# Kernel tuning notes

Measured on AMD Instinct MI355X. Metric: run time of the kernel, lower is better.

Reference implementation:

```python
import jax, jax.numpy as jnp
import numpy as np

N, E, B = 20000, 60000, 512
F_IN, ED, H, C = 7, 3, 4, 256
HC = H * C  # 1024
D_MODEL = 1024
EPS_BN = 1e-5


def setup_inputs() -> dict:
    key = jax.random.key(0)
    ks = jax.random.split(key, 24)
    s = 0.05
    inp = {
        'x': jax.random.normal(ks[0], (N, F_IN), jnp.float32),
        'edge_index': jax.random.randint(ks[1], (2, E), 0, N, jnp.int32),
        'edge_attr': jax.random.normal(ks[2], (E, ED), jnp.float32),
        'batch': jnp.sort(jax.random.randint(ks[3], (N,), 0, B, jnp.int32)),
        'w0': jax.random.normal(ks[4], (F_IN, HC), jnp.float32) * s,
        'w_rest': jax.random.normal(ks[5], (3, HC, HC), jnp.float32) * s,
        'w_edge': jax.random.normal(ks[6], (4, ED, HC), jnp.float32) * s,
        'att_src': jax.random.normal(ks[7], (4, H, C), jnp.float32) * s,
        'att_dst': jax.random.normal(ks[8], (4, H, C), jnp.float32) * s,
        'att_edge': jax.random.normal(ks[9], (4, H, C), jnp.float32) * s,
        'bias012': jax.random.normal(ks[10], (3, HC), jnp.float32) * s,
        'bias3': jax.random.normal(ks[11], (C,), jnp.float32) * s,
        'bn_gamma': jnp.ones((3, HC), jnp.float32),
        'bn_beta': jnp.zeros((3, HC), jnp.float32),
        'bn_mean': jnp.zeros((3, HC), jnp.float32),
        'bn_var': jnp.ones((3, HC), jnp.float32),
        'gate_w': jax.random.normal(ks[12], (C, 1), jnp.float32) * s,
        'gate_b': jnp.zeros((1,), jnp.float32),
        'proj_w': jax.random.normal(ks[13], (C, D_MODEL), jnp.float32) * s,
        'proj_b': jnp.zeros((D_MODEL,), jnp.float32),
    }
    return inp


def _gat_layer(x, ei, ea, W, We, a_s, a_d, a_e, bias, concat):
    # PyG GATConv with edge_dim, add_self_loops=True (fill_value='mean'), eval mode (no dropout)
    n = x.shape[0]
    sl = jnp.arange(n, dtype=ei.dtype)
    ea_mean = ea.mean(axis=0)
    ei = jnp.concatenate([ei, jnp.stack([sl, sl])], axis=1)            # [2, E+N]
    ea = jnp.concatenate([ea, jnp.broadcast_to(ea_mean, (n, ea.shape[1]))], axis=0)
    h = (x @ W).reshape(n, H, C)                                       # [N,H,C]
    alpha_src = jnp.einsum('nhc,hc->nh', h, a_s)
    alpha_dst = jnp.einsum('nhc,hc->nh', h, a_d)
    eh = (ea @ We).reshape(-1, H, C)
    alpha_e = jnp.einsum('ehc,hc->eh', eh, a_e)
    src, dst = ei[0], ei[1]
    alpha = jax.nn.leaky_relu(alpha_src[src] + alpha_dst[dst] + alpha_e, 0.2)  # [E+N,H]
    amax = jax.ops.segment_max(alpha, dst, num_segments=n)
    alpha = jnp.exp(alpha - amax[dst])
    denom = jax.ops.segment_sum(alpha, dst, num_segments=n)
    alpha = alpha / (denom[dst] + 1e-16)
    msg = h[src] * alpha[:, :, None]                                   # [E+N,H,C]
    out = jax.ops.segment_sum(msg, dst, num_segments=n)                # [N,H,C]
    out = out.reshape(n, H * C) if concat else out.mean(axis=1)
    return out + bias


def reference(x, edge_index, edge_attr, batch, w0, w_rest, w_edge, att_src, att_dst,
              att_edge, bias012, bias3, bn_gamma, bn_beta, bn_mean, bn_var,
              gate_w, gate_b, proj_w, proj_b):
    h = x
    for i in range(4):
        W = w0 if i == 0 else w_rest[i - 1]
        concat = i < 3
        b = bias012[i] if concat else bias3
        h = _gat_layer(h, edge_index, edge_attr, W, w_edge[i],
                       att_src[i], att_dst[i], att_edge[i], b, concat)
        if i < 3:
            # BatchNorm1d in eval mode, then ReLU (dropout is identity in eval)
            h = (h - bn_mean[i]) * (bn_gamma[i] / jnp.sqrt(bn_var[i] + EPS_BN)) + bn_beta[i]
            h = jax.nn.relu(h)
    # AttentionalAggregation: segment softmax over gate scores, weighted sum per graph
    gate = h @ gate_w + gate_b                                         # [N,1]
    gmax = jax.ops.segment_max(gate, batch, num_segments=B)
    g = jnp.exp(gate - gmax[batch])
    gsum = jax.ops.segment_sum(g, batch, num_segments=B)
    w = g / (gsum[batch] + 1e-16)
    graph = jax.ops.segment_sum(w * h, batch, num_segments=B)          # [B,256]
    return graph @ proj_w + proj_b                                     # [B,1024]
```

## Files before the change

kernel.cpp:

```cpp
#include <hip/hip_runtime.h>
#include <math.h>

#define NN 20000
#define NP 20480
#define EE 60000
#define BB 512
#define HC 1024
#define HH 4
#define CC 256

typedef _Float16 f16;
typedef f16 half8 __attribute__((ext_vector_type(8)));
typedef f16 f16x4 __attribute__((ext_vector_type(4)));
typedef float floatx4 __attribute__((ext_vector_type(4)));
typedef float floatx16 __attribute__((ext_vector_type(16)));

__device__ __forceinline__ size_t af_off(int n, int c) {
    int mblk = n >> 7, rr = n & 127;
    int iter = c >> 5, kc = c & 31;
    int kh = kc >> 4, kg = (kc >> 3) & 1, e = kc & 7;
    return ((((size_t)(mblk * 32 + iter) * 2 + kh) * 4 + (rr >> 5)) * 64 +
            (kg * 32 + (rr & 31))) * 8 + e;
}

__global__ void ehist_kernel(const float* __restrict__ ea, const int* __restrict__ ei,
                             float* sums, int* counts, int E_) {
    int e = blockIdx.x * 256 + threadIdx.x;
    float s0 = 0.f, s1 = 0.f, s2 = 0.f;
    if (e < E_) {
        atomicAdd(&counts[ei[E_ + e]], 1);
        s0 = ea[e * 3 + 0];
        s1 = ea[e * 3 + 1];
        s2 = ea[e * 3 + 2];
    }
    for (int o = 32; o; o >>= 1) {
        s0 += __shfl_down(s0, o);
        s1 += __shfl_down(s1, o);
        s2 += __shfl_down(s2, o);
    }
    if ((threadIdx.x & 63) == 0) {
        atomicAdd(&sums[0], s0);
        atomicAdd(&sums[1], s1);
        atomicAdd(&sums[2], s2);
    }
}

__global__ void scan1_kernel(const int* __restrict__ counts, int* __restrict__ partial,
                             int* __restrict__ psums, int n) {
    __shared__ int sdata[256];
    int t = threadIdx.x;
    int i = blockIdx.x * 256 + t;
    int v = (i < n) ? counts[i] : 0;
    sdata[t] = v;
    __syncthreads();
#pragma unroll
    for (int off = 1; off < 256; off <<= 1) {
        int tmp = (t >= off) ? sdata[t - off] : 0;
        __syncthreads();
        sdata[t] += tmp;
        __syncthreads();
    }
    if (i < n) partial[i] = sdata[t];
    if (t == 255) psums[blockIdx.x] = sdata[255];
}

__global__ void scan2_kernel(int* __restrict__ psums, int nb) {
    __shared__ int sdata[128];
    int t = threadIdx.x;
    sdata[t] = (t < nb) ? psums[t] : 0;
    __syncthreads();
#pragma unroll
    for (int off = 1; off < 128; off <<= 1) {
        int tmp = (t >= off) ? sdata[t - off] : 0;
        __syncthreads();
        sdata[t] += tmp;
        __syncthreads();
    }
    if (t < nb) psums[t] = (t == 0) ? 0 : sdata[t - 1];
}

__global__ void scan3_kernel(const int* __restrict__ partial, const int* __restrict__ psums,
                             int* __restrict__ indptr, int n) {
    int i = blockIdx.x * 256 + threadIdx.x;
    if (i == 0) indptr[0] = 0;
    if (i < n) indptr[i + 1] = partial[i] + psums[blockIdx.x];
}

__global__ void scatter_kernel(const int* __restrict__ ei, const int* __restrict__ indptr,
                               int* fill, int* sorted, int* sdst, int E_) {
    int e = blockIdx.x * 256 + threadIdx.x;
    if (e >= E_) return;
    int d = ei[E_ + e];
    int pos = indptr[d] + atomicAdd(&fill[d], 1);
    sorted[pos] = e;
    sdst[pos] = d;
}

__global__ void bptr_kernel(const int* __restrict__ batch, int* bptr, int n, int nb) {
    int i = blockIdx.x * 256 + threadIdx.x;
    if (i >= n) return;
    int b = batch[i];
    if (i == 0) {
        for (int bb = 0; bb <= b; bb++) bptr[bb] = 0;
    } else {
        int pb = batch[i - 1];
        if (pb != b) {
            for (int bb = pb + 1; bb <= b; bb++) bptr[bb] = i;
        }
    }
    if (i == n - 1) {
        for (int bb = b + 1; bb <= nb; bb++) bptr[bb] = n;
    }
}

__global__ void prep0_kernel(const float* __restrict__ w_rest, f16* __restrict__ Bf,
                             const float* __restrict__ att_src,
                             const float* __restrict__ att_dst,
                             const float* __restrict__ w0,
                             const float* __restrict__ bias012, const float* __restrict__ bn_g,
                             const float* __restrict__ bn_b, const float* __restrict__ bn_m,
                             const float* __restrict__ bn_v,
                             const float* __restrict__ w_edge,
                             const float* __restrict__ att_edge,
                             const float* __restrict__ ea_sums,
                             float* __restrict__ wsv, float* __restrict__ wdv,
                             float* __restrict__ w0s, float* __restrict__ w0d,
                             float2* __restrict__ bnss,
                             float* __restrict__ Mmat, float* __restrict__ ae_self,
                             float invE) {
    int bid = blockIdx.x;
    int t = threadIdx.x;
    if (bid < 768) {
        __shared__ float tile[64][65];
        int bx = (bid & 15) * 64;
        int by = ((bid >> 4) & 15) * 64;
        int l = bid >> 8;
        int tr = t >> 6, tc = t & 63;
#pragma unroll
        for (int i = 0; i < 16; i++) {
            int r = by + i * 4 + tr;
            tile[i * 4 + tr][tc] = w_rest[(size_t)l * 1048576 + (size_t)r * 1024 + bx + tc];
        }
        __syncthreads();
        f16* bl = Bf + (size_t)l * 1048576;
#pragma unroll
        for (int ii = 0; ii < 2; ii++) {
            int idx = ii * 256 + t;
            int nl = idx >> 3, kg8 = idx & 7;
            int n = bx + nl, k = by + kg8 * 8;
            half8 v;
#pragma unroll
            for (int e = 0; e < 8; e++) v[e] = (f16)tile[kg8 * 8 + e][nl];
            *(half8*)&bl[af_off(n, k)] = v;
        }
    } else if (bid < 3840) {
        int b = bid - 768;
        int l = b >> 10, k = b & 1023;
        int hp = t >> 6, lane = t & 63;
        int col = hp * 256 + lane * 4;
        const float* wrow = w_rest + (size_t)l * 1048576 + (size_t)k * 1024;
        float4 w4 = *(const float4*)&wrow[col];
        float4 a4 = *(const float4*)&att_src[(l + 1) * HC + col];
        float4 d4 = *(const float4*)&att_dst[(l + 1) * HC + col];
        float sp = w4.x * a4.x + w4.y * a4.y + w4.z * a4.z + w4.w * a4.w;
        float dp = w4.x * d4.x + w4.y * d4.y + w4.z * d4.z + w4.w * d4.w;
        for (int m = 1; m < 64; m <<= 1) {
            sp += __shfl_xor(sp, m);
            dp += __shfl_xor(dp, m);
        }
        if (lane == 0) {
            wsv[((size_t)l * 1024 + k) * 4 + hp] = sp;
            wdv[((size_t)l * 1024 + k) * 4 + hp] = dp;
        }
    } else if (bid < 3847) {
        int f = bid - 3840;
        int hp = t >> 6, lane = t & 63;
        int col = hp * 256 + lane * 4;
        float4 w4 = *(const float4*)&w0[f * HC + col];
        float4 a4 = *(const float4*)&att_src[col];
        float4 d4 = *(const float4*)&att_dst[col];
        float sp = w4.x * a4.x + w4.y * a4.y + w4.z * a4.z + w4.w * a4.w;
        float dp = w4.x * d4.x + w4.y * d4.y + w4.z * d4.z + w4.w * d4.w;
        for (int m = 1; m < 64; m <<= 1) {
            sp += __shfl_xor(sp, m);
            dp += __shfl_xor(dp, m);
        }
        if (lane == 0) {
            w0s[f * 4 + hp] = sp;
            w0d[f * 4 + hp] = dp;
        }
    } else if (bid < 3859) {
        int i = (bid - 3847) * 256 + t;
        if (i < 3 * HC) {
            float s = bn_g[i] * rsqrtf(bn_v[i] + 1e-5f);
            float2 o;
            o.x = s;
            o.y = (bias012[i] - bn_m[i]) * s + bn_b[i];
            bnss[i] = o;
        }
    } else {
        __shared__ float red[256];
        __shared__ float Ms[12];
        int l = bid - 3859;
        for (int dh = 0; dh < 12; dh++) {
            int d = dh >> 2, hh = dh & 3;
            float v = w_edge[l * 3072 + d * HC + hh * CC + t] *
                      att_edge[l * HC + hh * CC + t];
            red[t] = v;
            __syncthreads();
            for (int o = 128; o; o >>= 1) {
                if (t < o) red[t] += red[t + o];
                __syncthreads();
            }
            if (t == 0) {
                Ms[dh] = red[0];
                Mmat[l * 12 + dh] = red[0];
            }
            __syncthreads();
        }
        if (t < 4) {
            float v = 0.f;
            for (int d = 0; d < 3; d++) v += ea_sums[d] * invE * Ms[d * 4 + t];
            ae_self[l * 4 + t] = v;
        }
    }
}

__global__ void prep2_kernel(const int* __restrict__ ei, const int* __restrict__ sorted,
                             const float* __restrict__ ea, const float* __restrict__ Mmat,
                             int* __restrict__ ssrc, float* __restrict__ aeh_pk,
                             const float* __restrict__ x, const float* __restrict__ w0s,
                             const float* __restrict__ w0d, float* __restrict__ asrc,
                             float* __restrict__ adst, float* __restrict__ xpad) {
    int bid = blockIdx.x;
    int t = threadIdx.x;
    if (bid < 235) {
        int idx = bid * 256 + t;
        if (idx >= EE) return;
        int eid = sorted[idx];
        ssrc[idx] = ei[eid];
        float a0 = ea[eid * 3 + 0], a1 = ea[eid * 3 + 1], a2 = ea[eid * 3 + 2];
#pragma unroll
        for (int l = 0; l < 4; l++) {
#pragma unroll
            for (int h = 0; h < 4; h++) {
                aeh_pk[(size_t)idx * 16 + l * 4 + h] =
                    a0 * Mmat[l * 12 + h] + a1 * Mmat[l * 12 + 4 + h] +
                    a2 * Mmat[l * 12 + 8 + h];
            }
        }
    } else {
        int n = (bid - 235) * 256 + t;
        if (n >= NN) return;
        float xr[7];
#pragma unroll
        for (int f = 0; f < 7; f++) xr[f] = x[n * 7 + f];
        float4 p0, p1;
        p0.x = xr[0]; p0.y = xr[1]; p0.z = xr[2]; p0.w = xr[3];
        p1.x = xr[4]; p1.y = xr[5]; p1.z = xr[6]; p1.w = 0.f;
        *(float4*)&xpad[(size_t)n * 8] = p0;
        *(float4*)&xpad[(size_t)n * 8 + 4] = p1;
#pragma unroll
        for (int hp = 0; hp < 4; hp++) {
            float s = 0.f, d = 0.f;
#pragma unroll
            for (int f = 0; f < 7; f++) {
                s += xr[f] * w0s[f * 4 + hp];
                d += xr[f] * w0d[f * 4 + hp];
            }
            asrc[n * 4 + hp] = s;
            adst[n * 4 + hp] = d;
        }
    }
}

__global__ void edgep_kernel(const int* __restrict__ ssrc, const int* __restrict__ sdst,
                             const float* __restrict__ aeh_pk, const float* __restrict__ asrc,
                             const float* __restrict__ adst, float* __restrict__ pe,
                             int layer) {
    int i = blockIdx.x * 256 + threadIdx.x;
    if (i >= EE) return;
    int src = ssrc[i];
    int dst = sdst[i];
    float4 a = *(const float4*)&asrc[(size_t)src * 4];
    float4 d = *(const float4*)&adst[(size_t)dst * 4];
    float4 m = *(const float4*)&aeh_pk[(size_t)i * 16 + layer * 4];
    float r[4] = {a.x + d.x + m.x, a.y + d.y + m.y, a.z + d.z + m.z, a.w + d.w + m.w};
    float4 o;
#pragma unroll
    for (int k = 0; k < 4; k++) {
        float v = (r[k] > 0.f) ? r[k] : 0.2f * r[k];
        (&o.x)[k] = __expf(v);
    }
    *(float4*)&pe[(size_t)i * 4] = o;
}

__global__ void agg0x_kernel(const float* __restrict__ xpad, const float* __restrict__ asrc,
                             const float* __restrict__ adst, const float* __restrict__ ae_self,
                             const int* __restrict__ ssrc, const float* __restrict__ pe,
                             const int* __restrict__ indptr, float* __restrict__ xagg) {
    int n = blockIdx.x * 256 + threadIdx.x;
    if (n >= NN) return;
    float4 as4 = *(const float4*)&asrc[(size_t)n * 4];
    float4 ad4 = *(const float4*)&adst[(size_t)n * 4];
    float adl[4] = {ad4.x, ad4.y, ad4.z, ad4.w};
    float asl[4] = {as4.x, as4.y, as4.z, as4.w};
    float4 x0 = *(const float4*)&xpad[(size_t)n * 8];
    float4 x1 = *(const float4*)&xpad[(size_t)n * 8 + 4];
    float xr[7] = {x0.x, x0.y, x0.z, x0.w, x1.x, x1.y, x1.z};
    float denom[4];
    float xa[4][7];
#pragma unroll
    for (int h = 0; h < 4; h++) {
        float r = asl[h] + adl[h] + ae_self[h];
        r = (r > 0.f) ? r : 0.2f * r;
        float p = __expf(r);
        denom[h] = p;
#pragma unroll
        for (int f = 0; f < 7; f++) xa[h][f] = p * xr[f];
    }
    int s = indptr[n], e = indptr[n + 1];
    for (int idx = s; idx < e; idx++) {
        int src = ssrc[idx];
        float4 pv = *(const float4*)&pe[(size_t)idx * 4];
        float pl[4] = {pv.x, pv.y, pv.z, pv.w};
        float4 s0 = *(const float4*)&xpad[(size_t)src * 8];
        float4 s1 = *(const float4*)&xpad[(size_t)src * 8 + 4];
        float xs[7] = {s0.x, s0.y, s0.z, s0.w, s1.x, s1.y, s1.z};
#pragma unroll
        for (int h = 0; h < 4; h++) {
            denom[h] += pl[h];
#pragma unroll
            for (int f = 0; f < 7; f++) xa[h][f] += pl[h] * xs[f];
        }
    }
#pragma unroll
    for (int h = 0; h < 4; h++) {
        float inv = 1.0f / (denom[h] + 1e-16f);
#pragma unroll
        for (int f = 0; f < 7; f++) xagg[(size_t)n * 28 + h * 7 + f] = xa[h][f] * inv;
    }
}

__global__ void gemm7f_kernel(const float* __restrict__ xagg, const float* __restrict__ w0,
                              const float2* __restrict__ bnss, const float* __restrict__ wsv,
                              const float* __restrict__ wdv, f16* __restrict__ outAf,
                              float* __restrict__ asrc_n, float* __restrict__ adst_n) {
    __shared__ float xs[28];
    __shared__ float red[32];
    int n = blockIdx.x, t = threadIdx.x;
    if (t < 28) xs[t] = xagg[(size_t)n * 28 + t];
    __syncthreads();
    int head = t >> 6;
    int j0 = t * 4;
    float sp[4] = {0.f, 0.f, 0.f, 0.f}, dp[4] = {0.f, 0.f, 0.f, 0.f};
    f16x4 o;
#pragma unroll
    for (int k = 0; k < 4; k++) {
        int j = j0 + k;
        float dot = 0.f;
#pragma unroll
        for (int f = 0; f < 7; f++) dot += xs[head * 7 + f] * w0[f * HC + j];
        float2 ss = bnss[j];
        float val = fmaxf(fmaf(dot, ss.x, ss.y), 0.f);
        o[k] = (f16)val;
        float4 w4s = *(const float4*)&wsv[(size_t)j * 4];
        float4 w4d = *(const float4*)&wdv[(size_t)j * 4];
        sp[0] += val * w4s.x; sp[1] += val * w4s.y;
        sp[2] += val * w4s.z; sp[3] += val * w4s.w;
        dp[0] += val * w4d.x; dp[1] += val * w4d.y;
        dp[2] += val * w4d.z; dp[3] += val * w4d.w;
    }
    *(f16x4*)&outAf[af_off(n, j0)] = o;
    int wave = t >> 6, lane = t & 63;
#pragma unroll
    for (int m = 1; m < 64; m <<= 1) {
#pragma unroll
        for (int j = 0; j < 4; j++) {
            sp[j] += __shfl_xor(sp[j], m);
            dp[j] += __shfl_xor(dp[j], m);
        }
    }
    if (lane == 0) {
#pragma unroll
        for (int j = 0; j < 4; j++) {
            red[wave * 8 + j] = sp[j];
            red[wave * 8 + 4 + j] = dp[j];
        }
    }
    __syncthreads();
    if (t < 8) {
        float v = red[t] + red[8 + t] + red[16 + t] + red[24 + t];
        if (t < 4) asrc_n[n * 4 + t] = v;
        else adst_n[n * 4 + (t - 4)] = v;
    }
}

#define EPB 235
__global__ __launch_bounds__(256) void gemmep_kernel(
    const f16* __restrict__ Af, const f16* __restrict__ Bf, f16* __restrict__ C16,
    const int* __restrict__ ssrc, const int* __restrict__ sdst,
    const float* __restrict__ aeh_pk, const float* __restrict__ asrc,
    const float* __restrict__ adst, float* __restrict__ pe, int layer) {
    int t = threadIdx.x;
    int bid = blockIdx.x;
    if (bid < EPB) {
        int i = bid * 256 + t;
        if (i >= EE) return;
        int src = ssrc[i];
        int dst = sdst[i];
        float4 a = *(const float4*)&asrc[(size_t)src * 4];
        float4 d = *(const float4*)&adst[(size_t)dst * 4];
        float4 m = *(const float4*)&aeh_pk[(size_t)i * 16 + layer * 4];
        float r[4] = {a.x + d.x + m.x, a.y + d.y + m.y, a.z + d.z + m.z, a.w + d.w + m.w};
        float4 o;
#pragma unroll
        for (int k = 0; k < 4; k++) {
            float v = (r[k] > 0.f) ? r[k] : 0.2f * r[k];
            (&o.x)[k] = __expf(v);
        }
        *(float4*)&pe[(size_t)i * 4] = o;
        return;
    }
    int gid = bid - EPB;
    int wave = t >> 6, lane = t & 63;
    int g = gid >> 6, rblk = gid & 63;
    int nblk = rblk >> 3;
    int mblk = g * 8 + (rblk & 7);
    int rg0 = (wave >> 1) * 2;
    int cg0 = (wave & 1) * 2;

    floatx16 acc[2][2];
#pragma unroll
    for (int i = 0; i < 2; i++)
#pragma unroll
        for (int j = 0; j < 2; j++) acc[i][j] = (floatx16)(0.f);

    const f16* pa = Af + (size_t)mblk * 131072 + (size_t)lane * 8;
    const f16* pb = Bf + (size_t)nblk * 131072 + (size_t)lane * 8;

#pragma unroll 2
    for (int iter = 0; iter < 32; iter++) {
        size_t base = (size_t)iter * 4096;
        half8 afr[2][2], bfr[2][2];
#pragma unroll
        for (int kh = 0; kh < 2; kh++) {
#pragma unroll
            for (int i = 0; i < 2; i++) {
                afr[kh][i] = *(const half8*)&pa[base + kh * 2048 + (rg0 + i) * 512];
                bfr[kh][i] = *(const half8*)&pb[base + kh * 2048 + (cg0 + i) * 512];
            }
        }
#pragma unroll
        for (int kh = 0; kh < 2; kh++)
#pragma unroll
            for (int i = 0; i < 2; i++)
#pragma unroll
                for (int j = 0; j < 2; j++)
                    acc[i][j] = __builtin_amdgcn_mfma_f32_32x32x16_f16(bfr[kh][j], afr[kh][i],
                                                                       acc[i][j], 0, 0, 0);
    }

    int fr32 = lane & 31, kg = lane >> 5;
#pragma unroll
    for (int i = 0; i < 2; i++) {
        int row = mblk * 128 + rg0 * 32 + i * 32 + fr32;
#pragma unroll
        for (int j = 0; j < 2; j++) {
#pragma unroll
            for (int gq = 0; gq < 4; gq++) {
                f16x4 o;
#pragma unroll
                for (int r = 0; r < 4; r++) o[r] = (f16)acc[i][j][gq * 4 + r];
                *(f16x4*)&C16[(size_t)row * HC + nblk * 128 + cg0 * 32 + j * 32 + gq * 8 +
                              kg * 4] = o;
            }
        }
    }
}

__global__ void agg_kernel(const f16* __restrict__ h16, const float* __restrict__ asrc,
                           const float* __restrict__ adst, const float* __restrict__ ae_self,
                           const int* __restrict__ ssrc, const float* __restrict__ pe,
                           const int* __restrict__ indptr, const float2* __restrict__ bnss,
                           const float* __restrict__ wsv, const float* __restrict__ wdv,
                           const float* __restrict__ bias3, const float* __restrict__ gw,
                           const float* __restrict__ gb, f16* __restrict__ out16,
                           float* __restrict__ asrc_n, float* __restrict__ adst_n,
                           float* __restrict__ out3, float* __restrict__ gate,
                           int layer, int concat) {
    __shared__ float buf[1024];
    __shared__ float red[32];
    int n = blockIdx.x, t = threadIdx.x;
    int h = t >> 6, lane = t & 63;
    int c4 = t * 4;

    float r = asrc[n * 4 + h] + adst[n * 4 + h] + ae_self[layer * 4 + h];
    r = (r > 0.f) ? r : 0.2f * r;
    float p = __expf(r);
    float denom = p;
    float ax, ay, az, aw;
    {
        f16x4 v = *(const f16x4*)&h16[(size_t)n * HC + c4];
        ax = p * (float)v[0]; ay = p * (float)v[1];
        az = p * (float)v[2]; aw = p * (float)v[3];
    }
    int s = indptr[n], epos = indptr[n + 1];
    for (int base = s; base < epos; base += 4) {
        int rem = epos - base;
        int src[4];
        float pv[4];
#pragma unroll
        for (int j = 0; j < 4; j++) {
            if (j < rem) {
                src[j] = ssrc[base + j];
                pv[j] = pe[(size_t)(base + j) * 4 + h];
            } else {
                src[j] = n;
                pv[j] = 0.f;
            }
        }
        f16x4 u[4];
#pragma unroll
        for (int j = 0; j < 4; j++) u[j] = *(const f16x4*)&h16[(size_t)src[j] * HC + c4];
#pragma unroll
        for (int j = 0; j < 4; j++) {
            denom += pv[j];
            ax += pv[j] * (float)u[j][0];
            ay += pv[j] * (float)u[j][1];
            az += pv[j] * (float)u[j][2];
            aw += pv[j] * (float)u[j][3];
        }
    }
    float inv = 1.0f / (denom + 1e-16f);
    ax *= inv; ay *= inv; az *= inv; aw *= inv;

    if (concat) {
        float vals[4] = {ax, ay, az, aw};
        f16x4 o;
        float sp[4] = {0.f, 0.f, 0.f, 0.f}, dp[4] = {0.f, 0.f, 0.f, 0.f};
#pragma unroll
        for (int k = 0; k < 4; k++) {
            int j = c4 + k;
            float2 ss = bnss[j];
            float val = fmaxf(fmaf(vals[k], ss.x, ss.y), 0.f);
            o[k] = (f16)val;
            float4 w4s = *(const float4*)&wsv[(size_t)j * 4];
            float4 w4d = *(const float4*)&wdv[(size_t)j * 4];
            sp[0] += val * w4s.x; sp[1] += val * w4s.y;
            sp[2] += val * w4s.z; sp[3] += val * w4s.w;
            dp[0] += val * w4d.x; dp[1] += val * w4d.y;
            dp[2] += val * w4d.z; dp[3] += val * w4d.w;
        }
        *(f16x4*)&out16[af_off(n, c4)] = o;
#pragma unroll
        for (int m = 1; m < 64; m <<= 1) {
#pragma unroll
            for (int j = 0; j < 4; j++) {
                sp[j] += __shfl_xor(sp[j], m);
                dp[j] += __shfl_xor(dp[j], m);
            }
        }
        if (lane == 0) {
#pragma unroll
            for (int j = 0; j < 4; j++) {
                red[h * 8 + j] = sp[j];
                red[h * 8 + 4 + j] = dp[j];
            }
        }
        __syncthreads();
        if (t < 8) {
            float v = red[t] + red[8 + t] + red[16 + t] + red[24 + t];
            if (t < 4) asrc_n[n * 4 + t] = v;
            else adst_n[n * 4 + (t - 4)] = v;
        }
    } else {
        buf[c4 + 0] = ax;
        buf[c4 + 1] = ay;
        buf[c4 + 2] = az;
        buf[c4 + 3] = aw;
        __syncthreads();
        if (t < 64) {
            float gpart = 0.f;
#pragma unroll
            for (int k = 0; k < 4; k++) {
                int c = t * 4 + k;
                float v2 = 0.25f * (buf[c] + buf[256 + c] + buf[512 + c] + buf[768 + c]) +
                           bias3[c];
                out3[(size_t)n * CC + c] = v2;
                gpart += v2 * gw[c];
            }
            for (int o = 32; o; o >>= 1) gpart += __shfl_down(gpart, o);
            if (t == 0) gate[n] = gpart + gb[0];
        }
    }
}

__global__ void graphagg_kernel(const float* __restrict__ gate, const float* __restrict__ h3,
                                const int* __restrict__ bptr, float* __restrict__ graph) {
    __shared__ float red[256];
    __shared__ float wn[256];
    int b = blockIdx.x, t = threadIdx.x;
    int s = bptr[b], epos = bptr[b + 1];
    float m = -3.4e38f;
    for (int n = s + t; n < epos; n += 256) m = fmaxf(m, gate[n]);
    red[t] = m;
    __syncthreads();
    for (int o = 128; o; o >>= 1) {
        if (t < o) red[t] = fmaxf(red[t], red[t + o]);
        __syncthreads();
    }
    float mval = red[0];
    __syncthreads();
    float sum = 0.f;
    for (int n = s + t; n < epos; n += 256) sum += __expf(gate[n] - mval);
    red[t] = sum;
    __syncthreads();
    for (int o = 128; o; o >>= 1) {
        if (t < o) red[t] += red[t + o];
        __syncthreads();
    }
    float ssum = red[0];
    __syncthreads();
    float acc = 0.f;
    for (int base = s; base < epos; base += 256) {
        int n = base + t;
        wn[t] = (n < epos) ? __expf(gate[n] - mval) : 0.f;
        __syncthreads();
        int cnt = min(256, epos - base);
        for (int j = 0; j < cnt; j++) acc += wn[j] * h3[(size_t)(base + j) * CC + t];
        __syncthreads();
    }
    graph[b * CC + t] = acc / (ssum + 1e-16f);
}

__global__ void proj_kernel(const float* __restrict__ graph, const float* __restrict__ pw,
                            const float* __restrict__ pb, float* __restrict__ out) {
    __shared__ float g[8][256];
    int b = blockIdx.x, t = threadIdx.x;
#pragma unroll
    for (int r = 0; r < 8; r++) g[r][t] = graph[(size_t)(b * 8 + r) * 256 + t];
    __syncthreads();
    float acc[8][4];
#pragma unroll
    for (int r = 0; r < 8; r++)
#pragma unroll
        for (int q = 0; q < 4; q++) acc[r][q] = pb[t + q * 256];
    for (int c = 0; c < 256; c++) {
        float w[4];
#pragma unroll
        for (int q = 0; q < 4; q++) w[q] = pw[(size_t)c * 1024 + t + q * 256];
#pragma unroll
        for (int r = 0; r < 8; r++) {
            float gv = g[r][c];
#pragma unroll
            for (int q = 0; q < 4; q++) acc[r][q] += gv * w[q];
        }
    }
#pragma unroll
    for (int r = 0; r < 8; r++)
#pragma unroll
        for (int q = 0; q < 4; q++)
            out[(size_t)(b * 8 + r) * 1024 + t + q * 256] = acc[r][q];
}

extern "C" void kernel_launch(void* const* d_in, const int* in_sizes, int n_in,
                              void* d_out, int out_size, void* d_ws, size_t ws_size,
                              hipStream_t stream) {
    const float* x = (const float*)d_in[0];
    const int* ei = (const int*)d_in[1];
    const float* ea = (const float*)d_in[2];
    const int* batch = (const int*)d_in[3];
    const float* w0 = (const float*)d_in[4];
    const float* w_rest = (const float*)d_in[5];
    const float* w_edge = (const float*)d_in[6];
    const float* att_src = (const float*)d_in[7];
    const float* att_dst = (const float*)d_in[8];
    const float* att_edge = (const float*)d_in[9];
    const float* bias012 = (const float*)d_in[10];
    const float* bias3 = (const float*)d_in[11];
    const float* bn_g = (const float*)d_in[12];
    const float* bn_b = (const float*)d_in[13];
    const float* bn_m = (const float*)d_in[14];
    const float* bn_v = (const float*)d_in[15];
    const float* gate_w = (const float*)d_in[16];
    const float* gate_b = (const float*)d_in[17];
    const float* proj_w = (const float*)d_in[18];
    const float* proj_b = (const float*)d_in[19];
    float* out = (float*)d_out;

    float* ws = (float*)d_ws;
    size_t off = 0;
    f16* h_lin = (f16*)(ws + off); off += (size_t)NP * HC / 2;
    f16* h_af = (f16*)(ws + off); off += (size_t)NP * HC / 2;
    float* h3 = ws + off; off += (size_t)NN * CC;
    f16* Bf = (f16*)(ws + off); off += (size_t)3 * HC * HC / 2;
    float* xpad = ws + off; off += (size_t)NN * 8;
    float* asrcA = ws + off; off += (size_t)NN * 4;
    float* adstA = ws + off; off += (size_t)NN * 4;
    float* asrcB = ws + off; off += (size_t)NN * 4;
    float* adstB = ws + off; off += (size_t)NN * 4;
    float* wsv = ws + off; off += (size_t)3 * HC * 4;
    float* wdv = ws + off; off += (size_t)3 * HC * 4;
    float* w0s = ws + off; off += 28;
    float* w0d = ws + off; off += 28;
    float2* bnss = (float2*)(ws + off); off += (size_t)3 * HC * 2;
    float* aeh_pk = ws + off; off += (size_t)EE * 16;
    float* pbuf = ws + off; off += (size_t)EE * 4;
    float* xagg = ws + off; off += (size_t)NN * 28;
    float* gate = ws + off; off += (size_t)NN;
    float* graph = ws + off; off += (size_t)BB * CC;
    float* ea_sums = ws + off; off += 4;
    float* Mmat = ws + off; off += 48;
    float* ae_self = ws + off; off += 16;
    int* counts = (int*)(ws + off); off += NN;
    int* partial = (int*)(ws + off); off += NN;
    int* psums = (int*)(ws + off); off += 128;
    int* indptr = (int*)(ws + off); off += NN + 1;
    int* fill = (int*)(ws + off); off += NN;
    int* sorted = (int*)(ws + off); off += EE;
    int* ssrc = (int*)(ws + off); off += EE;
    int* sdst = (int*)(ws + off); off += EE;
    int* bptr = (int*)(ws + off); off += BB + 1;

    hipMemsetAsync(ea_sums, 0, 4 * sizeof(float), stream);
    hipMemsetAsync(counts, 0, NN * sizeof(int), stream);
    hipMemsetAsync(fill, 0, NN * sizeof(int), stream);

    ehist_kernel<<<(EE + 255) / 256, 256, 0, stream>>>(ea, ei, ea_sums, counts, EE);
    int nblk = (NN + 255) / 256;
    scan1_kernel<<<nblk, 256, 0, stream>>>(counts, partial, psums, NN);
    scan2_kernel<<<1, 128, 0, stream>>>(psums, nblk);
    scan3_kernel<<<nblk, 256, 0, stream>>>(partial, psums, indptr, NN);
    scatter_kernel<<<(EE + 255) / 256, 256, 0, stream>>>(ei, indptr, fill, sorted, sdst, EE);
    bptr_kernel<<<(NN + 255) / 256, 256, 0, stream>>>(batch, bptr, NN, BB);
    prep0_kernel<<<3863, 256, 0, stream>>>(w_rest, Bf, att_src, att_dst, w0, bias012, bn_g,
                                           bn_b, bn_m, bn_v, w_edge, att_edge, ea_sums,
                                           wsv, wdv, w0s, w0d, bnss, Mmat, ae_self,
                                           1.0f / EE);
    prep2_kernel<<<235 + nblk, 256, 0, stream>>>(ei, sorted, ea, Mmat, ssrc, aeh_pk,
                                                 x, w0s, w0d, asrcA, adstA, xpad);

    edgep_kernel<<<(EE + 255) / 256, 256, 0, stream>>>(ssrc, sdst, aeh_pk, asrcA, adstA,
                                                       pbuf, 0);
    agg0x_kernel<<<nblk, 256, 0, stream>>>(xpad, asrcA, adstA, ae_self, ssrc,
                                           pbuf, indptr, xagg);
    gemm7f_kernel<<<NN, 256, 0, stream>>>(xagg, w0, bnss, wsv, wdv, h_af, asrcB, adstB);

    float* asrc_cur = asrcB;
    float* adst_cur = adstB;
    float* asrc_nxt = asrcA;
    float* adst_nxt = adstA;
    for (int i = 1; i < 4; i++) {
        gemmep_kernel<<<EPB + (NP / 128) * (HC / 128), 256, 0, stream>>>(
            h_af, Bf + (size_t)(i - 1) * HC * HC, h_lin,
            ssrc, sdst, aeh_pk, asrc_cur, adst_cur, pbuf, i);
        agg_kernel<<<NN, 256, 0, stream>>>(
            h_lin, asrc_cur, adst_cur, ae_self, ssrc, pbuf, indptr, bnss + (size_t)i * HC,
            wsv + (size_t)i * HC * 4, wdv + (size_t)i * HC * 4, bias3, gate_w, gate_b,
            h_af, asrc_nxt, adst_nxt, h3, gate, i, (i < 3) ? 1 : 0);
        float* tmp = asrc_cur; asrc_cur = asrc_nxt; asrc_nxt = tmp;
        tmp = adst_cur; adst_cur = adst_nxt; adst_nxt = tmp;
    }

    graphagg_kernel<<<BB, 256, 0, stream>>>(gate, h3, bptr, graph);
    proj_kernel<<<BB / 8, 256, 0, stream>>>(graph, proj_w, proj_b, out);
}
```

Before: 681.7 us.

## Stage GEMM tiles through double-buffered LDS with direct global-to-LDS loads

The fused GEMM part of gemmep_kernel now copies each K-step's A and B fragments into shared memory with global_load_lds, and each wave loads a quarter of the tile instead of every wave reading its own fragments straight from global memory. Two LDS buffers alternate so the next tile's load is issued before the current tile's MFMAs run. The goal is to cut redundant global reads, since A and B fragments are shared across waves, and to hide load latency. In exchange it adds 32KB of LDS per block and two barriers per iteration. The barriers may not wait for the async LDS loads to complete (no explicit vmcnt wait), so correctness depends on the compiler's waitcnt insertion.

```diff
diff --git a/kernel.cpp b/kernel.cpp
--- a/kernel.cpp
+++ b/kernel.cpp
@@ -21,6 +21,11 @@
     int kh = kc >> 4, kg = (kc >> 3) & 1, e = kc & 7;
     return ((((size_t)(mblk * 32 + iter) * 2 + kh) * 4 + (rr >> 5)) * 64 +
             (kg * 32 + (rr & 31))) * 8 + e;
+}
+
+__device__ __forceinline__ void gload16(const f16* g, f16* l) {
+    __builtin_amdgcn_global_load_lds((const __attribute__((address_space(1))) void*)g,
+                                     (__attribute__((address_space(3))) void*)l, 16, 0, 0);
 }
 
 __global__ void ehist_kernel(const float* __restrict__ ea, const int* __restrict__ ei,
@@ -402,6 +407,7 @@
     const int* __restrict__ ssrc, const int* __restrict__ sdst,
     const float* __restrict__ aeh_pk, const float* __restrict__ asrc,
     const float* __restrict__ adst, float* __restrict__ pe, int layer) {
+    __shared__ __align__(16) f16 lds[16384];
     int t = threadIdx.x;
     int bid = blockIdx.x;
     if (bid < EPB) {
@@ -423,12 +429,12 @@
         return;
     }
     int gid = bid - EPB;
-    int wave = t >> 6, lane = t & 63;
+    int w = t >> 6, lane = t & 63;
     int g = gid >> 6, rblk = gid & 63;
     int nblk = rblk >> 3;
     int mblk = g * 8 + (rblk & 7);
-    int rg0 = (wave >> 1) * 2;
-    int cg0 = (wave & 1) * 2;
+    int rg0 = (w >> 1) * 2;
+    int cg0 = (w & 1) * 2;
 
     floatx16 acc[2][2];
 #pragma unroll
@@ -436,19 +442,29 @@
 #pragma unroll
         for (int j = 0; j < 2; j++) acc[i][j] = (floatx16)(0.f);
 
-    const f16* pa = Af + (size_t)mblk * 131072 + (size_t)lane * 8;
-    const f16* pb = Bf + (size_t)nblk * 131072 + (size_t)lane * 8;
-
-#pragma unroll 2
-    for (int iter = 0; iter < 32; iter++) {
-        size_t base = (size_t)iter * 4096;
+    const f16* ga0 = Af + (size_t)mblk * 131072 + w * 1024 + lane * 8;
+    const f16* gb0 = Bf + (size_t)nblk * 131072 + w * 1024 + lane * 8;
+
+    auto STAGE = [&](int it, int b) {
+        const f16* ga = ga0 + (size_t)it * 4096;
+        const f16* gb = gb0 + (size_t)it * 4096;
+        f16* la = &lds[b * 8192 + w * 1024 + lane * 8];
+        f16* lb = &lds[b * 8192 + 4096 + w * 1024 + lane * 8];
+        gload16(ga, la);
+        gload16(ga + 512, la + 512);
+        gload16(gb, lb);
+        gload16(gb + 512, lb + 512);
+    };
+    auto COMPUTE = [&](int b) {
         half8 afr[2][2], bfr[2][2];
 #pragma unroll
         for (int kh = 0; kh < 2; kh++) {
 #pragma unroll
             for (int i = 0; i < 2; i++) {
-                afr[kh][i] = *(const half8*)&pa[base + kh * 2048 + (rg0 + i) * 512];
-                bfr[kh][i] = *(const half8*)&pb[base + kh * 2048 + (cg0 + i) * 512];
+                afr[kh][i] = *(const half8*)&lds[b * 8192 + kh * 2048 + (rg0 + i) * 512 +
+                                                 lane * 8];
+                bfr[kh][i] = *(const half8*)&lds[b * 8192 + 4096 + kh * 2048 +
+                                                 (cg0 + i) * 512 + lane * 8];
             }
         }
 #pragma unroll
@@ -459,6 +475,19 @@
                 for (int j = 0; j < 2; j++)
                     acc[i][j] = __builtin_amdgcn_mfma_f32_32x32x16_f16(bfr[kh][j], afr[kh][i],
                                                                        acc[i][j], 0, 0, 0);
+    };
+
+    STAGE(0, 0);
+    __syncthreads();
+#pragma unroll 1
+    for (int k2 = 0; k2 < 16; k2++) {
+        int i0 = k2 * 2;
+        STAGE(i0 + 1, 1);
+        COMPUTE(0);
+        __syncthreads();
+        if (i0 + 2 < 32) STAGE(i0 + 2, 0);
+        COMPUTE(1);
+        __syncthreads();
     }
 
     int fr32 = lane & 31, kg = lane >> 5;
```

Measured after the change: 649.5 us. -4.7%, faster.
